# Kernel tuning notes

Hardware: AMD Instinct MI355X
Metric: run time of the kernel (lower is better)

The kernel has to match this reference:

```python
import jax, jax.numpy as jnp
import numpy as np

N, INC, INN = 8, 32, 50000
OUTC, OUTN, D = 64, 8192, 32  # D = uniform neighbor count (maxD)


def setup_inputs() -> dict:
    key = jax.random.key(0)
    k1, k2, k3, k4, k5 = jax.random.split(key, 5)
    x = jax.random.normal(k1, (N, INC, INN), dtype=jnp.float32)
    nf_weight = jax.random.normal(k2, (INC, INN), dtype=jnp.float32)
    # torch init: uniform(-1,1) * sqrt(6/(1+5*inc)); exact distribution irrelevant for correctness baseline
    ft_weight = (jax.random.uniform(k3, (INC, OUTC), dtype=jnp.float32) * 2.0 - 1.0) * np.sqrt(6.0 / (1.0 + 5 * INC)).astype(np.float32)
    bias = 0.2 * jax.random.normal(k4, (OUTC, OUTN), dtype=jnp.float32)
    A = jax.random.randint(k5, (OUTN, D), 0, INN, dtype=jnp.int32)
    return {"x": x, "nf_weight": nf_weight, "ft_weight": ft_weight, "bias": bias, "A": A}


def reference(x, nf_weight, ft_weight, bias, A):
    # op_order '132': (1) node/feature weight on input, (3) gather+max reduce, (2) feature transform
    y = x * nf_weight                      # (N, inc, inn)
    gathered = y[:, :, A]                  # (N, inc, outn, D) -- padded adjacency gather
    red = jnp.max(gathered, axis=-1)       # (N, inc, outn)    -- reduction='max', mask all-ones (uniform degree)
    out = jnp.einsum('nio,ik->nko', red, ft_weight)  # (N, outc, outn)
    return out + bias                      # bias (outc, outn) broadcast over N
```

## Files before the change

### kernel.cpp

```cpp
#include <hip/hip_runtime.h>
#include <math.h>

#define NN   8
#define INCH 32
#define INN  50000
#define OUTC 64
#define OUTN 8192
#define DD   32
#define CC   256

typedef unsigned short ushortT;

__device__ __forceinline__ ushortT f2bf(float f) {
  unsigned u = __float_as_uint(f);
  unsigned r = (u + 0x7FFFu + ((u >> 16) & 1u)) >> 16;
  return (ushortT)r;
}
__device__ __forceinline__ float bf2f(ushortT b) {
  return __uint_as_float(((unsigned)b) << 16);
}

__global__ __launch_bounds__(256) void prep_kernel(
    const float* __restrict__ x, const float* __restrict__ nf, ushortT* __restrict__ yT) {
  __shared__ ushortT tile[CC][34];
  const int t = threadIdx.x;
  const int j0 = blockIdx.x * 32;
  const int jmax = min(32, INN - j0);

  const int q  = t & 7;
  const int r0 = t >> 3;

  if (q * 4 < jmax) {
    const float4 nv = *(const float4*)(nf + (size_t)r0 * INN + j0 + 4 * q);
    #pragma unroll
    for (int p = 0; p < 8; ++p) {
      const int c = (p << 5) + r0;
      const float4 xv = *(const float4*)(x + (size_t)c * INN + j0 + 4 * q);
      const unsigned w0 = ((unsigned)f2bf(xv.y * nv.y) << 16) | (unsigned)f2bf(xv.x * nv.x);
      const unsigned w1 = ((unsigned)f2bf(xv.w * nv.w) << 16) | (unsigned)f2bf(xv.z * nv.z);
      *(unsigned*)&tile[c][4 * q]     = w0;
      *(unsigned*)&tile[c][4 * q + 2] = w1;
    }
  }
  __syncthreads();

  const int lane = t & 63;
  const int wave = t >> 6;
  #pragma unroll
  for (int r = 0; r < 8; ++r) {
    const int jl = wave * 8 + r;
    if (jl < jmax) {
      ushort4 pk;
      pk.x = tile[lane][jl];
      pk.y = tile[64 + lane][jl];
      pk.z = tile[128 + lane][jl];
      pk.w = tile[192 + lane][jl];
      ((ushort4*)(yT + (size_t)(j0 + jl) * CC))[lane] = pk;
    }
  }
}

__global__ __launch_bounds__(256) void gather_kernel(
    const ushortT* __restrict__ yT, const int* __restrict__ A, ushortT* __restrict__ red16) {
  const int t = threadIdx.x;
  const int lane = t & 63;
  const int wave = t >> 6;
  const int o = blockIdx.x * 4 + wave;

  const int4* A4 = (const int4*)(A + (size_t)o * DD);
  int4 id[8];
  #pragma unroll
  for (int q = 0; q < 8; ++q) id[q] = A4[q];

  float a0 = -INFINITY, a1 = -INFINITY, a2 = -INFINITY, a3 = -INFINITY;
  #pragma unroll
  for (int q = 0; q < 8; ++q) {
    int ids[4] = {id[q].x, id[q].y, id[q].z, id[q].w};
    #pragma unroll
    for (int e = 0; e < 4; ++e) {
      const ushort4 v = ((const ushort4*)(yT + (size_t)ids[e] * CC))[lane];
      a0 = fmaxf(a0, bf2f(v.x));
      a1 = fmaxf(a1, bf2f(v.y));
      a2 = fmaxf(a2, bf2f(v.z));
      a3 = fmaxf(a3, bf2f(v.w));
    }
  }
  ushortT* ro = red16 + (size_t)o * CC + lane;
  ro[0]   = f2bf(a0);
  ro[64]  = f2bf(a1);
  ro[128] = f2bf(a2);
  ro[192] = f2bf(a3);
}

__global__ __launch_bounds__(256) void out_kernel(
    const ushortT* __restrict__ red16, const float* __restrict__ ft,
    const float* __restrict__ bias, float* __restrict__ out) {
  __shared__ float rtile[64][65];
  __shared__ float ftl[32][64];
  const int t = threadIdx.x;
  const int lane = t & 63;
  const int wave = t >> 6;
  const int np = blockIdx.x >> 7;
  const int ot = blockIdx.x & 127;
  const int o0 = ot * 64;
  const int c0 = np * 64;

  #pragma unroll
  for (int q = 0; q < 8; ++q) {
    const int idx = q * 256 + t;
    ftl[idx >> 6][idx & 63] = ft[idx];
  }
  #pragma unroll
  for (int i = 0; i < 2; ++i) {
    const int r = (t >> 3) + 32 * i;
    const int g = t & 7;
    const ushort4* src = (const ushort4*)(red16 + (size_t)(o0 + r) * CC + c0 + g * 8);
    const ushort4 v0 = src[0];
    const ushort4 v1 = src[1];
    float* dst = &rtile[r][g * 8];
    dst[0] = bf2f(v0.x); dst[1] = bf2f(v0.y); dst[2] = bf2f(v0.z); dst[3] = bf2f(v0.w);
    dst[4] = bf2f(v1.x); dst[5] = bf2f(v1.y); dst[6] = bf2f(v1.z); dst[7] = bf2f(v1.w);
  }
  __syncthreads();

  const int n  = np * 2 + (wave & 1);
  const int kh = (wave >> 1) * 32;
  const int cb = (wave & 1) * 32;

  float rv[32];
  #pragma unroll
  for (int i = 0; i < 32; ++i) rv[i] = rtile[lane][cb + i];

  float acc[32];
  #pragma unroll
  for (int kk = 0; kk < 32; ++kk) acc[kk] = 0.f;
  #pragma unroll
  for (int i = 0; i < 32; ++i) {
    #pragma unroll
    for (int kk = 0; kk < 32; ++kk)
      acc[kk] += rv[i] * ftl[i][kh + kk];
  }

  float* op = out + (size_t)n * OUTC * OUTN + o0 + lane;
  const float* bp = bias + o0 + lane;
  #pragma unroll
  for (int kk = 0; kk < 32; ++kk) {
    const int k = kh + kk;
    op[(size_t)k * OUTN] = acc[kk] + bp[(size_t)k * OUTN];
  }
}

extern "C" void kernel_launch(void* const* d_in, const int* in_sizes, int n_in,
                              void* d_out, int out_size, void* d_ws, size_t ws_size,
                              hipStream_t stream) {
  const float* x    = (const float*)d_in[0];
  const float* nf   = (const float*)d_in[1];
  const float* ft   = (const float*)d_in[2];
  const float* bias = (const float*)d_in[3];
  const int*   A    = (const int*)d_in[4];
  float* out = (float*)d_out;

  ushortT* yT    = (ushortT*)d_ws;
  ushortT* red16 = (ushortT*)((char*)d_ws + (size_t)INN * CC * 2);

  hipLaunchKernelGGL(prep_kernel,   dim3((INN + 31) / 32), dim3(256), 0, stream, x, nf, yT);
  hipLaunchKernelGGL(gather_kernel, dim3(OUTN / 4),        dim3(256), 0, stream, yT, A, red16);
  hipLaunchKernelGGL(out_kernel,    dim3(512),             dim3(256), 0, stream, red16, ft, bias, out);
}
```

Measured before the change: 51.45 us.

## Interleave channel layout in yT so gather uses 16-byte loads per lane

The prep kernel now keeps float products in shared memory and writes yT with channels interleaved, so each group of 8 consecutive bf16 values holds channels c, c+32, ..., c+224. The gather kernel splits each wave into two half-waves that serve two output nodes, and each lane does one 16-byte load per neighbor in place of an 8-byte load. This halves the number of load instructions and raises bytes per request in the latency-bound random gather. The cost is a doubled shared tile in prep and a per-lane select of the neighbor index.

Result: no change. 52.20 us (+1.5%).

```diff
diff --git a/kernel.cpp b/kernel.cpp
--- a/kernel.cpp
+++ b/kernel.cpp
@@ -20,9 +20,10 @@
   return __uint_as_float(((unsigned)b) << 16);
 }
 
+
 __global__ __launch_bounds__(256) void prep_kernel(
     const float* __restrict__ x, const float* __restrict__ nf, ushortT* __restrict__ yT) {
-  __shared__ ushortT tile[CC][34];
+  __shared__ float tile[CC][33];
   const int t = threadIdx.x;
   const int j0 = blockIdx.x * 32;
   const int jmax = min(32, INN - j0);
@@ -36,25 +37,26 @@
     for (int p = 0; p < 8; ++p) {
       const int c = (p << 5) + r0;
       const float4 xv = *(const float4*)(x + (size_t)c * INN + j0 + 4 * q);
-      const unsigned w0 = ((unsigned)f2bf(xv.y * nv.y) << 16) | (unsigned)f2bf(xv.x * nv.x);
-      const unsigned w1 = ((unsigned)f2bf(xv.w * nv.w) << 16) | (unsigned)f2bf(xv.z * nv.z);
-      *(unsigned*)&tile[c][4 * q]     = w0;
-      *(unsigned*)&tile[c][4 * q + 2] = w1;
+      float4 pr;
+      pr.x = xv.x * nv.x; pr.y = xv.y * nv.y; pr.z = xv.z * nv.z; pr.w = xv.w * nv.w;
+      *(float4*)&tile[c][4 * q] = pr;
     }
   }
   __syncthreads();
 
   const int lane = t & 63;
   const int wave = t >> 6;
+  const int chi = (lane & 1) * 4;
+  const int clo = lane >> 1;
   #pragma unroll
   for (int r = 0; r < 8; ++r) {
     const int jl = wave * 8 + r;
     if (jl < jmax) {
       ushort4 pk;
-      pk.x = tile[lane][jl];
-      pk.y = tile[64 + lane][jl];
-      pk.z = tile[128 + lane][jl];
-      pk.w = tile[192 + lane][jl];
+      pk.x = f2bf(tile[(chi + 0) * 32 + clo][jl]);
+      pk.y = f2bf(tile[(chi + 1) * 32 + clo][jl]);
+      pk.z = f2bf(tile[(chi + 2) * 32 + clo][jl]);
+      pk.w = f2bf(tile[(chi + 3) * 32 + clo][jl]);
       ((ushort4*)(yT + (size_t)(j0 + jl) * CC))[lane] = pk;
     }
   }
@@ -65,31 +67,42 @@
   const int t = threadIdx.x;
   const int lane = t & 63;
   const int wave = t >> 6;
-  const int o = blockIdx.x * 4 + wave;
+  const int opair = blockIdx.x * 8 + wave * 2;
+  const int half = lane >> 5;
+  const int l32  = lane & 31;
+  const int o = opair + half;
 
-  const int4* A4 = (const int4*)(A + (size_t)o * DD);
-  int4 id[8];
+  const int4* Aa = (const int4*)(A + (size_t)opair * DD);
+  const int4* Ab = (const int4*)(A + (size_t)(opair + 1) * DD);
+
+  float m[8];
   #pragma unroll
-  for (int q = 0; q < 8; ++q) id[q] = A4[q];
+  for (int e = 0; e < 8; ++e) m[e] = -INFINITY;
 
-  float a0 = -INFINITY, a1 = -INFINITY, a2 = -INFINITY, a3 = -INFINITY;
+  const ushortT* base = yT + (size_t)l32 * 8;
   #pragma unroll
-  for (int q = 0; q < 8; ++q) {
-    int ids[4] = {id[q].x, id[q].y, id[q].z, id[q].w};
+  for (int g = 0; g < 8; ++g) {
+    const int4 va = Aa[g];
+    const int4 vb = Ab[g];
+    const int ia[4] = {va.x, va.y, va.z, va.w};
+    const int ib[4] = {vb.x, vb.y, vb.z, vb.w};
     #pragma unroll
     for (int e = 0; e < 4; ++e) {
-      const ushort4 v = ((const ushort4*)(yT + (size_t)ids[e] * CC))[lane];
-      a0 = fmaxf(a0, bf2f(v.x));
-      a1 = fmaxf(a1, bf2f(v.y));
-      a2 = fmaxf(a2, bf2f(v.z));
-      a3 = fmaxf(a3, bf2f(v.w));
+      const int idx = half ? ib[e] : ia[e];
+      const uint4 v = *(const uint4*)(base + (size_t)idx * CC);
+      m[0] = fmaxf(m[0], __uint_as_float(v.x << 16));
+      m[1] = fmaxf(m[1], __uint_as_float(v.x & 0xffff0000u));
+      m[2] = fmaxf(m[2], __uint_as_float(v.y << 16));
+      m[3] = fmaxf(m[3], __uint_as_float(v.y & 0xffff0000u));
+      m[4] = fmaxf(m[4], __uint_as_float(v.z << 16));
+      m[5] = fmaxf(m[5], __uint_as_float(v.z & 0xffff0000u));
+      m[6] = fmaxf(m[6], __uint_as_float(v.w << 16));
+      m[7] = fmaxf(m[7], __uint_as_float(v.w & 0xffff0000u));
     }
   }
-  ushortT* ro = red16 + (size_t)o * CC + lane;
-  ro[0]   = f2bf(a0);
-  ro[64]  = f2bf(a1);
-  ro[128] = f2bf(a2);
-  ro[192] = f2bf(a3);
+  ushortT* ro = red16 + (size_t)o * CC + l32;
+  #pragma unroll
+  for (int e = 0; e < 8; ++e) ro[32 * e] = f2bf(m[e]);
 }
 
 __global__ __launch_bounds__(256) void out_kernel(
@@ -164,6 +177,6 @@
   ushortT* red16 = (ushortT*)((char*)d_ws + (size_t)INN * CC * 2);
 
   hipLaunchKernelGGL(prep_kernel,   dim3((INN + 31) / 32), dim3(256), 0, stream, x, nf, yT);
-  hipLaunchKernelGGL(gather_kernel, dim3(OUTN / 4),        dim3(256), 0, stream, yT, A, red16);
+  hipLaunchKernelGGL(gather_kernel, dim3(OUTN / 8),        dim3(256), 0, stream, yT, A, red16);
   hipLaunchKernelGGL(out_kernel,    dim3(512),             dim3(256), 0, stream, red16, ft, bias, out);
 }
```

## Partition gather by source-index chunks with ballot-selected neighbors and partial maxima

Applied to the files above, without the earlier changes.

The gather kernel now splits the source-node range into 8 chunks. Each block handles only the neighbors whose index falls in its chunk, found with a wave ballot and readlane, so each block's working set of yT stays small enough to fit in cache. Per-chunk partial maxima are written with nontemporal stores to an 8x larger buffer, and the output kernel reduces them before the matmul. The prep kernel now holds fp32 in LDS and converts to bf16 when writing out. The cost is 8x more reduction-buffer traffic, serialized divergent loops over the ballot masks, and more reads in the output kernel.

New measurement: 68.87 us. 33.9% more time.

```diff
diff --git a/kernel.cpp b/kernel.cpp
--- a/kernel.cpp
+++ b/kernel.cpp
@@ -8,13 +8,14 @@
 #define OUTN 8192
 #define DD   32
 #define CC   256
+#define NCK  8
+#define CHUNK (INN / NCK)
 
 typedef unsigned short ushortT;
 
-__device__ __forceinline__ ushortT f2bf(float f) {
+__device__ __forceinline__ unsigned f2bf_u(float f) {
   unsigned u = __float_as_uint(f);
-  unsigned r = (u + 0x7FFFu + ((u >> 16) & 1u)) >> 16;
-  return (ushortT)r;
+  return (u + 0x7FFFu + ((u >> 16) & 1u)) >> 16;
 }
 __device__ __forceinline__ float bf2f(ushortT b) {
   return __uint_as_float(((unsigned)b) << 16);
@@ -22,7 +23,7 @@
 
 __global__ __launch_bounds__(256) void prep_kernel(
     const float* __restrict__ x, const float* __restrict__ nf, ushortT* __restrict__ yT) {
-  __shared__ ushortT tile[CC][34];
+  __shared__ float tile[CC][33];
   const int t = threadIdx.x;
   const int j0 = blockIdx.x * 32;
   const int jmax = min(32, INN - j0);
@@ -36,10 +37,9 @@
     for (int p = 0; p < 8; ++p) {
       const int c = (p << 5) + r0;
       const float4 xv = *(const float4*)(x + (size_t)c * INN + j0 + 4 * q);
-      const unsigned w0 = ((unsigned)f2bf(xv.y * nv.y) << 16) | (unsigned)f2bf(xv.x * nv.x);
-      const unsigned w1 = ((unsigned)f2bf(xv.w * nv.w) << 16) | (unsigned)f2bf(xv.z * nv.z);
-      *(unsigned*)&tile[c][4 * q]     = w0;
-      *(unsigned*)&tile[c][4 * q + 2] = w1;
+      float4 pr;
+      pr.x = xv.x * nv.x; pr.y = xv.y * nv.y; pr.z = xv.z * nv.z; pr.w = xv.w * nv.w;
+      *(float4*)&tile[c][4 * q] = pr;
     }
   }
   __syncthreads();
@@ -50,50 +50,75 @@
   for (int r = 0; r < 8; ++r) {
     const int jl = wave * 8 + r;
     if (jl < jmax) {
-      ushort4 pk;
-      pk.x = tile[lane][jl];
-      pk.y = tile[64 + lane][jl];
-      pk.z = tile[128 + lane][jl];
-      pk.w = tile[192 + lane][jl];
-      ((ushort4*)(yT + (size_t)(j0 + jl) * CC))[lane] = pk;
+      unsigned* dst = (unsigned*)(yT + (size_t)(j0 + jl) * CC);
+      #pragma unroll
+      for (int e = 0; e < 2; ++e) {
+        const int c0 = 128 * e + 2 * lane;
+        const unsigned lo = f2bf_u(tile[c0][jl]);
+        const unsigned hi = f2bf_u(tile[c0 + 1][jl]);
+        dst[lane + 64 * e] = lo | (hi << 16);
+      }
     }
   }
 }
 
 __global__ __launch_bounds__(256) void gather_kernel(
-    const ushortT* __restrict__ yT, const int* __restrict__ A, ushortT* __restrict__ red16) {
+    const ushortT* __restrict__ yT, const int* __restrict__ A, ushortT* __restrict__ redp) {
   const int t = threadIdx.x;
   const int lane = t & 63;
   const int wave = t >> 6;
-  const int o = blockIdx.x * 4 + wave;
-
-  const int4* A4 = (const int4*)(A + (size_t)o * DD);
-  int4 id[8];
-  #pragma unroll
-  for (int q = 0; q < 8; ++q) id[q] = A4[q];
-
-  float a0 = -INFINITY, a1 = -INFINITY, a2 = -INFINITY, a3 = -INFINITY;
-  #pragma unroll
-  for (int q = 0; q < 8; ++q) {
-    int ids[4] = {id[q].x, id[q].y, id[q].z, id[q].w};
-    #pragma unroll
-    for (int e = 0; e < 4; ++e) {
-      const ushort4 v = ((const ushort4*)(yT + (size_t)ids[e] * CC))[lane];
-      a0 = fmaxf(a0, bf2f(v.x));
-      a1 = fmaxf(a1, bf2f(v.y));
-      a2 = fmaxf(a2, bf2f(v.z));
-      a3 = fmaxf(a3, bf2f(v.w));
-    }
-  }
-  ushortT* ro = red16 + (size_t)o * CC + lane;
-  ro[0]   = f2bf(a0);
-  ro[64]  = f2bf(a1);
-  ro[128] = f2bf(a2);
-  ro[192] = f2bf(a3);
+  const int ck = blockIdx.x & 7;
+  const int ob = blockIdx.x >> 3;
+  const int jlo = ck * CHUNK, jhi = jlo + CHUNK;
+  const int o0 = ob * 64 + wave * 16;
+
+  #pragma unroll
+  for (int p = 0; p < 8; ++p) {
+    const int opair = o0 + 2 * p;
+    const int vidx = A[(size_t)opair * DD + lane];
+    const unsigned long long bal = __ballot(vidx >= jlo && vidx < jhi);
+    unsigned mlo = (unsigned)bal;
+    unsigned mhi = (unsigned)(bal >> 32);
+
+    float a0 = -INFINITY, a1 = -INFINITY, a2 = -INFINITY, a3 = -INFINITY;
+    float b0 = -INFINITY, b1 = -INFINITY, b2 = -INFINITY, b3 = -INFINITY;
+
+    while (mlo) {
+      const int bpos = __builtin_ctz(mlo); mlo &= mlo - 1;
+      const int sidx = __builtin_amdgcn_readlane(vidx, bpos);
+      const uint2 v = *(const uint2*)(yT + (size_t)sidx * CC + 4 * lane);
+      a0 = fmaxf(a0, __uint_as_float(v.x << 16));
+      a1 = fmaxf(a1, __uint_as_float(v.x & 0xffff0000u));
+      a2 = fmaxf(a2, __uint_as_float(v.y << 16));
+      a3 = fmaxf(a3, __uint_as_float(v.y & 0xffff0000u));
+    }
+    while (mhi) {
+      const int bpos = __builtin_ctz(mhi); mhi &= mhi - 1;
+      const int sidx = __builtin_amdgcn_readlane(vidx, bpos + 32);
+      const uint2 v = *(const uint2*)(yT + (size_t)sidx * CC + 4 * lane);
+      b0 = fmaxf(b0, __uint_as_float(v.x << 16));
+      b1 = fmaxf(b1, __uint_as_float(v.x & 0xffff0000u));
+      b2 = fmaxf(b2, __uint_as_float(v.y << 16));
+      b3 = fmaxf(b3, __uint_as_float(v.y & 0xffff0000u));
+    }
+
+    const unsigned long long ua =
+        (unsigned long long)(f2bf_u(a0) | (f2bf_u(a1) << 16)) |
+        ((unsigned long long)(f2bf_u(a2) | (f2bf_u(a3) << 16)) << 32);
+    const unsigned long long ub =
+        (unsigned long long)(f2bf_u(b0) | (f2bf_u(b1) << 16)) |
+        ((unsigned long long)(f2bf_u(b2) | (f2bf_u(b3) << 16)) << 32);
+    unsigned long long* r0 =
+        (unsigned long long*)(redp + ((size_t)ck * OUTN + opair) * CC) + lane;
+    unsigned long long* r1 =
+        (unsigned long long*)(redp + ((size_t)ck * OUTN + opair + 1) * CC) + lane;
+    __builtin_nontemporal_store(ua, r0);
+    __builtin_nontemporal_store(ub, r1);
+  }
 }
 
 __global__ __launch_bounds__(256) void out_kernel(
-    const ushortT* __restrict__ red16, const float* __restrict__ ft,
+    const ushortT* __restrict__ redp, const float* __restrict__ ft,
     const float* __restrict__ bias, float* __restrict__ out) {
   __shared__ float rtile[64][65];
   __shared__ float ftl[32][64];
@@ -114,12 +139,23 @@
   for (int i = 0; i < 2; ++i) {
     const int r = (t >> 3) + 32 * i;
     const int g = t & 7;
-    const ushort4* src = (const ushort4*)(red16 + (size_t)(o0 + r) * CC + c0 + g * 8);
-    const ushort4 v0 = src[0];
-    const ushort4 v1 = src[1];
+    float vm[8];
+    #pragma unroll
+    for (int u = 0; u < 8; ++u) vm[u] = -INFINITY;
+    #pragma unroll
+    for (int ck = 0; ck < NCK; ++ck) {
+      const ushort4* src =
+          (const ushort4*)(redp + ((size_t)ck * OUTN + o0 + r) * CC + c0 + g * 8);
+      const ushort4 v0 = src[0];
+      const ushort4 v1 = src[1];
+      vm[0] = fmaxf(vm[0], bf2f(v0.x)); vm[1] = fmaxf(vm[1], bf2f(v0.y));
+      vm[2] = fmaxf(vm[2], bf2f(v0.z)); vm[3] = fmaxf(vm[3], bf2f(v0.w));
+      vm[4] = fmaxf(vm[4], bf2f(v1.x)); vm[5] = fmaxf(vm[5], bf2f(v1.y));
+      vm[6] = fmaxf(vm[6], bf2f(v1.z)); vm[7] = fmaxf(vm[7], bf2f(v1.w));
+    }
     float* dst = &rtile[r][g * 8];
-    dst[0] = bf2f(v0.x); dst[1] = bf2f(v0.y); dst[2] = bf2f(v0.z); dst[3] = bf2f(v0.w);
-    dst[4] = bf2f(v1.x); dst[5] = bf2f(v1.y); dst[6] = bf2f(v1.z); dst[7] = bf2f(v1.w);
+    #pragma unroll
+    for (int u = 0; u < 8; ++u) dst[u] = vm[u];
   }
   __syncthreads();
 
@@ -160,10 +196,10 @@
   const int*   A    = (const int*)d_in[4];
   float* out = (float*)d_out;
 
-  ushortT* yT    = (ushortT*)d_ws;
-  ushortT* red16 = (ushortT*)((char*)d_ws + (size_t)INN * CC * 2);
+  ushortT* yT   = (ushortT*)d_ws;
+  ushortT* redp = (ushortT*)((char*)d_ws + (size_t)INN * CC * 2);
 
   hipLaunchKernelGGL(prep_kernel,   dim3((INN + 31) / 32), dim3(256), 0, stream, x, nf, yT);
-  hipLaunchKernelGGL(gather_kernel, dim3(OUTN / 4),        dim3(256), 0, stream, yT, A, red16);
-  hipLaunchKernelGGL(out_kernel,    dim3(512),             dim3(256), 0, stream, red16, ft, bias, out);
-}
+  hipLaunchKernelGGL(gather_kernel, dim3((OUTN / 64) * NCK), dim3(256), 0, stream, yT, A, redp);
+  hipLaunchKernelGGL(out_kernel,    dim3(512),             dim3(256), 0, stream, redp, ft, bias, out);
+}
```

## Partition bf16 node table into channel planes for cache-local gather

Applied to the files above, without the earlier changes.

The bf16 intermediate is now stored as 8 channel planes of 64 bytes per node, each word packing channels c and c+128. The gather kernel is split by plane, so each block only touches one plane (about 3.2MB) and that plane can stay resident in cache. The gather also loads the adjacency rows for 64 outputs into shared memory and reads 16-byte vectors per lane instead of 8-byte ones. In exchange, each adjacency index is read eight times, more blocks are launched, and the output kernel needs a matching unpack step.

Measured after the change: 47.09 us. -8.5%, faster.

```diff
diff --git a/kernel.cpp b/kernel.cpp
--- a/kernel.cpp
+++ b/kernel.cpp
@@ -8,21 +8,20 @@
 #define OUTN 8192
 #define DD   32
 #define CC   256
+#define NPL  8
+#define PLDW ((size_t)INN * 16)
 
 typedef unsigned short ushortT;
 
-__device__ __forceinline__ ushortT f2bf(float f) {
+__device__ __forceinline__ unsigned f2bf_u(float f) {
   unsigned u = __float_as_uint(f);
-  unsigned r = (u + 0x7FFFu + ((u >> 16) & 1u)) >> 16;
-  return (ushortT)r;
-}
-__device__ __forceinline__ float bf2f(ushortT b) {
-  return __uint_as_float(((unsigned)b) << 16);
+  return (u + 0x7FFFu + ((u >> 16) & 1u)) >> 16;
 }
 
+
 __global__ __launch_bounds__(256) void prep_kernel(
-    const float* __restrict__ x, const float* __restrict__ nf, ushortT* __restrict__ yT) {
-  __shared__ ushortT tile[CC][34];
+    const float* __restrict__ x, const float* __restrict__ nf, unsigned* __restrict__ yTc) {
+  __shared__ float tile[CC][33];
   const int t = threadIdx.x;
   const int j0 = blockIdx.x * 32;
   const int jmax = min(32, INN - j0);
@@ -36,10 +35,9 @@
     for (int p = 0; p < 8; ++p) {
       const int c = (p << 5) + r0;
       const float4 xv = *(const float4*)(x + (size_t)c * INN + j0 + 4 * q);
-      const unsigned w0 = ((unsigned)f2bf(xv.y * nv.y) << 16) | (unsigned)f2bf(xv.x * nv.x);
-      const unsigned w1 = ((unsigned)f2bf(xv.w * nv.w) << 16) | (unsigned)f2bf(xv.z * nv.z);
-      *(unsigned*)&tile[c][4 * q]     = w0;
-      *(unsigned*)&tile[c][4 * q + 2] = w1;
+      float4 pr;
+      pr.x = xv.x * nv.x; pr.y = xv.y * nv.y; pr.z = xv.z * nv.z; pr.w = xv.w * nv.w;
+      *(float4*)&tile[c][4 * q] = pr;
     }
   }
   __syncthreads();
@@ -50,50 +48,63 @@
   for (int r = 0; r < 8; ++r) {
     const int jl = wave * 8 + r;
     if (jl < jmax) {
-      ushort4 pk;
-      pk.x = tile[lane][jl];
-      pk.y = tile[64 + lane][jl];
-      pk.z = tile[128 + lane][jl];
-      pk.w = tile[192 + lane][jl];
-      ((ushort4*)(yT + (size_t)(j0 + jl) * CC))[lane] = pk;
+      #pragma unroll
+      for (int e = 0; e < 2; ++e) {
+        const int clo = lane + 64 * e;
+        const unsigned lo = f2bf_u(tile[clo][jl]);
+        const unsigned hi = f2bf_u(tile[clo + 128][jl]);
+        const int pl  = clo >> 4;
+        const int pos = clo & 15;
+        yTc[(size_t)pl * PLDW + (size_t)(j0 + jl) * 16 + pos] = lo | (hi << 16);
+      }
     }
   }
 }
 
 __global__ __launch_bounds__(256) void gather_kernel(
-    const ushortT* __restrict__ yT, const int* __restrict__ A, ushortT* __restrict__ red16) {
+    const unsigned* __restrict__ yTc, const int* __restrict__ A, unsigned* __restrict__ red32) {
+  __shared__ int Al[64 * 33];
   const int t = threadIdx.x;
   const int lane = t & 63;
   const int wave = t >> 6;
-  const int o = blockIdx.x * 4 + wave;
+  const int ck = blockIdx.x & 7;
+  const int ob = blockIdx.x >> 3;
+  const int o0 = ob * 64;
 
-  const int4* A4 = (const int4*)(A + (size_t)o * DD);
-  int4 id[8];
   #pragma unroll
-  for (int q = 0; q < 8; ++q) id[q] = A4[q];
+  for (int k = 0; k < 8; ++k) {
+    const int f = k * 256 + t;
+    Al[(f >> 5) * 33 + (f & 31)] = A[(size_t)o0 * DD + f];
+  }
+  __syncthreads();
 
-  float a0 = -INFINITY, a1 = -INFINITY, a2 = -INFINITY, a3 = -INFINITY;
-  #pragma unroll
-  for (int q = 0; q < 8; ++q) {
-    int ids[4] = {id[q].x, id[q].y, id[q].z, id[q].w};
-    #pragma unroll
-    for (int e = 0; e < 4; ++e) {
-      const ushort4 v = ((const ushort4*)(yT + (size_t)ids[e] * CC))[lane];
-      a0 = fmaxf(a0, bf2f(v.x));
-      a1 = fmaxf(a1, bf2f(v.y));
-      a2 = fmaxf(a2, bf2f(v.z));
-      a3 = fmaxf(a3, bf2f(v.w));
-    }
+  const unsigned* plane = yTc + (size_t)ck * PLDW;
+  const int osub = wave * 16 + (lane >> 2);
+  const int cq   = lane & 3;
+
+  float l0 = -INFINITY, l1 = -INFINITY, l2 = -INFINITY, l3 = -INFINITY;
+  float h0 = -INFINITY, h1 = -INFINITY, h2 = -INFINITY, h3 = -INFINITY;
+
+  #pragma unroll 8
+  for (int d = 0; d < 32; ++d) {
+    const int idx = Al[osub * 33 + d];
+    const uint4 v = *(const uint4*)(plane + (size_t)idx * 16 + cq * 4);
+    l0 = fmaxf(l0, __uint_as_float(v.x << 16));  h0 = fmaxf(h0, __uint_as_float(v.x & 0xffff0000u));
+    l1 = fmaxf(l1, __uint_as_float(v.y << 16));  h1 = fmaxf(h1, __uint_as_float(v.y & 0xffff0000u));
+    l2 = fmaxf(l2, __uint_as_float(v.z << 16));  h2 = fmaxf(h2, __uint_as_float(v.z & 0xffff0000u));
+    l3 = fmaxf(l3, __uint_as_float(v.w << 16));  h3 = fmaxf(h3, __uint_as_float(v.w & 0xffff0000u));
   }
-  ushortT* ro = red16 + (size_t)o * CC + lane;
-  ro[0]   = f2bf(a0);
-  ro[64]  = f2bf(a1);
-  ro[128] = f2bf(a2);
-  ro[192] = f2bf(a3);
+
+  uint4 pk;
+  pk.x = (__float_as_uint(l0) >> 16) | (__float_as_uint(h0) & 0xffff0000u);
+  pk.y = (__float_as_uint(l1) >> 16) | (__float_as_uint(h1) & 0xffff0000u);
+  pk.z = (__float_as_uint(l2) >> 16) | (__float_as_uint(h2) & 0xffff0000u);
+  pk.w = (__float_as_uint(l3) >> 16) | (__float_as_uint(h3) & 0xffff0000u);
+  *(uint4*)(red32 + ((size_t)(o0 + osub) * 128) + ck * 16 + cq * 4) = pk;
 }
 
 __global__ __launch_bounds__(256) void out_kernel(
-    const ushortT* __restrict__ red16, const float* __restrict__ ft,
+    const unsigned* __restrict__ red32, const float* __restrict__ ft,
     const float* __restrict__ bias, float* __restrict__ out) {
   __shared__ float rtile[64][65];
   __shared__ float ftl[32][64];
@@ -103,7 +114,8 @@
   const int np = blockIdx.x >> 7;
   const int ot = blockIdx.x & 127;
   const int o0 = ot * 64;
-  const int c0 = np * 64;
+  const int hi = np >> 1;
+  const int sb = (np & 1) * 64;
 
   #pragma unroll
   for (int q = 0; q < 8; ++q) {
@@ -114,12 +126,14 @@
   for (int i = 0; i < 2; ++i) {
     const int r = (t >> 3) + 32 * i;
     const int g = t & 7;
-    const ushort4* src = (const ushort4*)(red16 + (size_t)(o0 + r) * CC + c0 + g * 8);
-    const ushort4 v0 = src[0];
-    const ushort4 v1 = src[1];
+    const unsigned* src = red32 + (size_t)(o0 + r) * 128 + sb + g * 8;
+    const uint4 v0 = *(const uint4*)(src);
+    const uint4 v1 = *(const uint4*)(src + 4);
+    const unsigned w[8] = {v0.x, v0.y, v0.z, v0.w, v1.x, v1.y, v1.z, v1.w};
     float* dst = &rtile[r][g * 8];
-    dst[0] = bf2f(v0.x); dst[1] = bf2f(v0.y); dst[2] = bf2f(v0.z); dst[3] = bf2f(v0.w);
-    dst[4] = bf2f(v1.x); dst[5] = bf2f(v1.y); dst[6] = bf2f(v1.z); dst[7] = bf2f(v1.w);
+    #pragma unroll
+    for (int u = 0; u < 8; ++u)
+      dst[u] = __uint_as_float(hi ? (w[u] & 0xffff0000u) : (w[u] << 16));
   }
   __syncthreads();
 
@@ -160,10 +174,10 @@
   const int*   A    = (const int*)d_in[4];
   float* out = (float*)d_out;
 
-  ushortT* yT    = (ushortT*)d_ws;
-  ushortT* red16 = (ushortT*)((char*)d_ws + (size_t)INN * CC * 2);
+  unsigned* yTc   = (unsigned*)d_ws;
+  unsigned* red32 = (unsigned*)((char*)d_ws + NPL * PLDW * 4);
 
-  hipLaunchKernelGGL(prep_kernel,   dim3((INN + 31) / 32), dim3(256), 0, stream, x, nf, yT);
-  hipLaunchKernelGGL(gather_kernel, dim3(OUTN / 4),        dim3(256), 0, stream, yT, A, red16);
-  hipLaunchKernelGGL(out_kernel,    dim3(512),             dim3(256), 0, stream, red16, ft, bias, out);
+  hipLaunchKernelGGL(prep_kernel,   dim3((INN + 31) / 32),  dim3(256), 0, stream, x, nf, yTc);
+  hipLaunchKernelGGL(gather_kernel, dim3((OUTN / 64) * NPL), dim3(256), 0, stream, yTc, A, red32);
+  hipLaunchKernelGGL(out_kernel,    dim3(512),              dim3(256), 0, stream, red32, ft, bias, out);
 }
```
